# Performance work log

Hardware: AMD Instinct MI355X
Metric: run time of the kernel (lower is better)

## Reference

```python
import jax, jax.numpy as jnp
import numpy as np

N_NODES = 100000
N_EDGES = 1600000
IN_FEAT = 64
HIDDEN = 128
N_CLASSES = 16
N_GRAPHS = 512


def _glorot(key, shape):
    fan_in, fan_out = shape
    lim = (6.0 / (fan_in + fan_out)) ** 0.5
    return jax.random.uniform(key, shape, jnp.float32, -lim, lim)


def setup_inputs() -> dict:
    key = jax.random.key(0)
    ks = jax.random.split(key, 12)
    x = jax.random.normal(ks[0], (N_NODES, IN_FEAT), jnp.float32)
    edge_index = jax.random.randint(ks[1], (2, N_EDGES), 0, N_NODES, jnp.int64)
    batch = jnp.sort(jax.random.randint(ks[2], (N_NODES,), 0, N_GRAPHS, jnp.int64))
    # SAGEConv params: lin_l (neighbor agg, with bias), lin_r (root, no bias)
    params = {}
    dims = [(IN_FEAT, HIDDEN), (HIDDEN, HIDDEN), (HIDDEN, HIDDEN)]
    for i, (din, dout) in enumerate(dims, start=1):
        params[f"Wl{i}"] = _glorot(ks[2 + 2 * i - 1], (din, dout))
        params[f"bl{i}"] = jnp.zeros((dout,), jnp.float32)
        params[f"Wr{i}"] = _glorot(ks[2 + 2 * i], (din, dout))
    params["W_out"] = _glorot(ks[9], (HIDDEN, N_CLASSES))
    params["b_out"] = jnp.zeros((N_CLASSES,), jnp.float32)
    return {"x": x, "edge_index": edge_index, "batch": batch, **params}


def _sage_conv(x, src, dst, Wl, bl, Wr):
    # mean aggregation of neighbor (source) features onto target nodes
    msg = x[src]                                                # [E, D]
    agg_sum = jax.ops.segment_sum(msg, dst, num_segments=N_NODES)
    cnt = jax.ops.segment_sum(jnp.ones((src.shape[0],), x.dtype), dst,
                              num_segments=N_NODES)
    agg = agg_sum / jnp.maximum(cnt, 1.0)[:, None]
    return agg @ Wl + bl + x @ Wr


def reference(x, edge_index, batch, Wl1, bl1, Wr1, Wl2, bl2, Wr2,
              Wl3, bl3, Wr3, W_out, b_out):
    src, dst = edge_index[0], edge_index[1]
    h = jax.nn.relu(_sage_conv(x, src, dst, Wl1, bl1, Wr1))
    h = jax.nn.relu(_sage_conv(h, src, dst, Wl2, bl2, Wr2))
    h = _sage_conv(h, src, dst, Wl3, bl3, Wr3)
    # global mean pool over graphs
    g_sum = jax.ops.segment_sum(h, batch, num_segments=N_GRAPHS)
    g_cnt = jax.ops.segment_sum(jnp.ones((h.shape[0],), h.dtype), batch,
                                num_segments=N_GRAPHS)
    g = g_sum / jnp.maximum(g_cnt, 1.0)[:, None]
    # dropout is identity at inference (module.eval())
    return g @ W_out + b_out
```

## Files before the change

kernel.cpp:

```cpp
#include <hip/hip_runtime.h>

#define N_NODES   100000
#define N_PAD     100096
#define N_EDGES   1600000
#define IN_FEAT   64
#define HIDDEN    128
#define N_CLASSES 16
#define N_GRAPHS  512
#define MAXDEG    64

#define BIN_NODES 512
#define NBINS     196
#define N_NODES_B (NBINS * BIN_NODES)
#define BINCAP    9000
#define EPB       2048

typedef __attribute__((ext_vector_type(8))) unsigned short us8;
typedef __attribute__((ext_vector_type(8))) short s8v;
typedef __attribute__((ext_vector_type(4))) float f4v;

__device__ __forceinline__ unsigned short f2bf(float f) {
    unsigned u = __builtin_bit_cast(unsigned, f);
    unsigned r = u + 0x7FFFu + ((u >> 16) & 1u);
    return (unsigned short)(r >> 16);
}
__device__ __forceinline__ float bf2f(unsigned short h) {
    unsigned u = ((unsigned)h) << 16;
    return __builtin_bit_cast(float, u);
}
__device__ __forceinline__ void acc8(float* a, us8 v) {
#pragma unroll
    for (int e = 0; e < 8; e++) a[e] += bf2f(v[e]);
}


__global__ __launch_bounds__(512) void bin_kernel(const int* __restrict__ src,
                                                  const int* __restrict__ dst,
                                                  int* __restrict__ bin_cursor,
                                                  int2* __restrict__ binbuf) {
    __shared__ int hist[NBINS];
    __shared__ int base[NBINS];
    const int t = threadIdx.x;
    for (int i = t; i < NBINS; i += 512) hist[i] = 0;
    __syncthreads();

    const int e0 = blockIdx.x * EPB;
    int myb[4], mys[4], myd[4], myp[4];
#pragma unroll
    for (int j = 0; j < 4; j++) {
        int e = e0 + t + j * 512;
        if (e < N_EDGES) {
            myd[j] = dst[e];
            mys[j] = src[e];
            myb[j] = myd[j] >> 9;
        } else {
            myb[j] = -1; mys[j] = 0; myd[j] = 0;
        }
    }
#pragma unroll
    for (int j = 0; j < 4; j++)
        myp[j] = (myb[j] >= 0) ? atomicAdd(&hist[myb[j]], 1) : 0;
    __syncthreads();

    for (int i = t; i < NBINS; i += 512) {
        int h = hist[i];
        base[i] = (h > 0) ? atomicAdd(&bin_cursor[i], h) : 0;
    }
    __syncthreads();

#pragma unroll
    for (int j = 0; j < 4; j++) {
        if (myb[j] >= 0) {
            int pos = base[myb[j]] + myp[j];
            if (pos < BINCAP)
                binbuf[(size_t)myb[j] * BINCAP + pos] = make_int2(mys[j], myd[j]);
        }
    }
}


__global__ __launch_bounds__(512) void build_kernel(const int2* __restrict__ binbuf,
                                                    const int* __restrict__ bin_cursor,
                                                    int* __restrict__ cursor,
                                                    int* __restrict__ csr) {
    __shared__ int lcur[BIN_NODES];
    __shared__ int lcsr[BIN_NODES * MAXDEG];
    const int b = blockIdx.x, t = threadIdx.x;
    if (t < BIN_NODES) lcur[t] = 0;
    __syncthreads();

    int cnt = bin_cursor[b];
    if (cnt > BINCAP) cnt = BINCAP;
    const int2* __restrict__ eb = binbuf + (size_t)b * BINCAP;
    for (int i = t; i < cnt; i += 512) {
        int2 e = eb[i];
        int dl = e.y - b * BIN_NODES;
        int p = atomicAdd(&lcur[dl], 1);
        if (p < MAXDEG) lcsr[dl * MAXDEG + p] = e.x;
    }
    __syncthreads();

    int4* __restrict__ gout = reinterpret_cast<int4*>(csr + (size_t)b * BIN_NODES * MAXDEG);
    const int4* __restrict__ lin = reinterpret_cast<const int4*>(lcsr);
    for (int i = t; i < BIN_NODES * MAXDEG / 4; i += 512) gout[i] = lin[i];
    if (t < BIN_NODES) cursor[b * BIN_NODES + t] = lcur[t];
}


__global__ void convert_x_kernel(const float* __restrict__ x, ushort* __restrict__ xh) {
    const int flat = blockIdx.x * 256 + threadIdx.x;
    const int row = flat >> 3;
    us8 w;
    if (row < N_NODES) {
        const float* p = x + (size_t)flat * 8;
        float4 v0 = *reinterpret_cast<const float4*>(p);
        float4 v1 = *reinterpret_cast<const float4*>(p + 4);
        w[0] = f2bf(v0.x); w[1] = f2bf(v0.y); w[2] = f2bf(v0.z); w[3] = f2bf(v0.w);
        w[4] = f2bf(v1.x); w[5] = f2bf(v1.y); w[6] = f2bf(v1.z); w[7] = f2bf(v1.w);
    } else {
#pragma unroll
        for (int e = 0; e < 8; e++) w[e] = 0;
    }
    reinterpret_cast<us8*>(xh)[flat] = w;
}


__global__ void pack_weights_kernel(const float* __restrict__ s0, const float* __restrict__ s1,
                                    const float* __restrict__ s2, const float* __restrict__ s3,
                                    const float* __restrict__ s4, const float* __restrict__ s5,
                                    ushort* __restrict__ Bpk) {
    const int flat = blockIdx.x * 256 + threadIdx.x;
    const float* src; int base;
    if      (flat < 8192)  { src = s0; base = 0; }
    else if (flat < 16384) { src = s1; base = 8192; }
    else if (flat < 32768) { src = s2; base = 16384; }
    else if (flat < 49152) { src = s3; base = 32768; }
    else if (flat < 65536) { src = s4; base = 49152; }
    else                   { src = s5; base = 65536; }
    const int local = flat - base;
    const int j    = local & 7;
    const int lane = (local >> 3) & 63;
    const int tile = local >> 9;
    const int ks = tile >> 3, ct = tile & 7;
    const int row = ks * 32 + ((lane >> 4) << 3) + j;
    const int col = (ct << 4) + (lane & 15);
    Bpk[flat] = f2bf(src[row * 128 + col]);
}


template <int D>
__global__ __launch_bounds__(256, 4) void aggregate_bf(
        const ushort* __restrict__ feat, const int* __restrict__ cursor,
        const int* __restrict__ csr, ushort* __restrict__ aggout) {
    constexpr int LPN = D / 8;
    constexpr int NPB = 256 / LPN;
    const int tid  = threadIdx.x;
    const int lane = tid & (LPN - 1);
    const int n    = blockIdx.x * NPB + tid / LPN;
    if (n >= N_NODES) return;
    const int start = n * MAXDEG;
    int cnt = cursor[n];
    if (cnt > MAXDEG) cnt = MAXDEG;
    const us8* __restrict__ f8 = reinterpret_cast<const us8*>(feat);

    float a[8] = {0.f, 0.f, 0.f, 0.f, 0.f, 0.f, 0.f, 0.f};
    int i = 0;
    for (; i + 16 <= cnt; i += 16) {
        int t[16];
#pragma unroll
        for (int u = 0; u < 16; u++) t[u] = csr[start + i + u];
        us8 v[16];
#pragma unroll
        for (int u = 0; u < 16; u++) v[u] = f8[(size_t)t[u] * LPN + lane];
#pragma unroll
        for (int u = 0; u < 16; u++) acc8(a, v[u]);
    }
    for (; i + 8 <= cnt; i += 8) {
        int t[8];
#pragma unroll
        for (int u = 0; u < 8; u++) t[u] = csr[start + i + u];
        us8 v[8];
#pragma unroll
        for (int u = 0; u < 8; u++) v[u] = f8[(size_t)t[u] * LPN + lane];
#pragma unroll
        for (int u = 0; u < 8; u++) acc8(a, v[u]);
    }
    for (; i + 4 <= cnt; i += 4) {
        int t0 = csr[start + i + 0], t1 = csr[start + i + 1];
        int t2 = csr[start + i + 2], t3 = csr[start + i + 3];
        us8 v0 = f8[(size_t)t0 * LPN + lane];
        us8 v1 = f8[(size_t)t1 * LPN + lane];
        us8 v2 = f8[(size_t)t2 * LPN + lane];
        us8 v3 = f8[(size_t)t3 * LPN + lane];
        acc8(a, v0); acc8(a, v1); acc8(a, v2); acc8(a, v3);
    }
    for (; i < cnt; i++) {
        us8 v0 = f8[(size_t)csr[start + i] * LPN + lane];
        acc8(a, v0);
    }
    const float inv = 1.f / (float)(cnt > 0 ? cnt : 1);
    us8 w;
#pragma unroll
    for (int e = 0; e < 8; e++) w[e] = f2bf(a[e] * inv);
    reinterpret_cast<us8*>(aggout)[(size_t)n * LPN + lane] = w;
}


template <int K, bool RELU>
__global__ __launch_bounds__(256, 2) void gemm_mfma(
        const ushort* __restrict__ A1, const ushort* __restrict__ A2,
        const ushort* __restrict__ B1p, const ushort* __restrict__ B2p,
        const float* __restrict__ bias, ushort* __restrict__ out) {
    constexpr int KS = K / 32;
    __shared__ ushort Bs[2 * KS * 8 * 512];
    const int tid = threadIdx.x;
    {
        const us8* g1 = reinterpret_cast<const us8*>(B1p);
        const us8* g2 = reinterpret_cast<const us8*>(B2p);
        us8* l8 = reinterpret_cast<us8*>(Bs);
        constexpr int PH = KS * 512;
#pragma unroll
        for (int i = 0; i < 4 * KS; i++) {
            int c = i * 256 + tid;
            if (i < 2 * KS) l8[c] = g1[c];
            else            l8[c] = g2[c - PH];
        }
    }
    __syncthreads();

    const int wave = tid >> 6, lane = tid & 63;
    const int r0 = blockIdx.x * 128 + wave * 32;
    const size_t arow = (size_t)(r0 + (lane & 15));
    const int koff = (lane >> 4) << 3;

    f4v acc[2][8];
#pragma unroll
    for (int rt = 0; rt < 2; rt++)
#pragma unroll
        for (int ct = 0; ct < 8; ct++) acc[rt][ct] = (f4v){0.f, 0.f, 0.f, 0.f};

    const s8v* Bf = reinterpret_cast<const s8v*>(Bs);
#pragma unroll
    for (int ph = 0; ph < 2; ph++) {
        const ushort* __restrict__ A = ph ? A2 : A1;
#pragma unroll
        for (int ks = 0; ks < KS; ks++) {
            s8v a0 = *reinterpret_cast<const s8v*>(A + arow * K + ks * 32 + koff);
            s8v a1 = *reinterpret_cast<const s8v*>(A + (arow + 16) * K + ks * 32 + koff);
#pragma unroll
            for (int ct = 0; ct < 8; ct++) {
                s8v b = Bf[((ph * KS + ks) * 8 + ct) * 64 + lane];
                acc[0][ct] = __builtin_amdgcn_mfma_f32_16x16x32_bf16(a0, b, acc[0][ct], 0, 0, 0);
                acc[1][ct] = __builtin_amdgcn_mfma_f32_16x16x32_bf16(a1, b, acc[1][ct], 0, 0, 0);
            }
        }
    }

    const int colb = lane & 15;
    const int rowb = (lane >> 4) << 2;
#pragma unroll
    for (int rt = 0; rt < 2; rt++) {
#pragma unroll
        for (int ct = 0; ct < 8; ct++) {
            const int col = ct * 16 + colb;
            const float bb = bias[col];
#pragma unroll
            for (int j = 0; j < 4; j++) {
                int row = r0 + rt * 16 + rowb + j;
                if (row < N_NODES) {
                    float v = acc[rt][ct][j] + bb;
                    if (RELU) v = fmaxf(v, 0.f);
                    out[(size_t)row * HIDDEN + col] = f2bf(v);
                }
            }
        }
    }
}


__global__ __launch_bounds__(256) void pool_bf(const ushort* __restrict__ h,
                                               const int* __restrict__ batch,
                                               float* __restrict__ g) {
    __shared__ int sb[5];
    const int g0 = blockIdx.x * 4;
    const int tid = threadIdx.x;
    if (tid <= 4) {
        int target = g0 + tid;
        int lo = 0, hi = N_NODES;
        while (lo < hi) {
            int mid = (lo + hi) >> 1;
            if (batch[mid] < target) lo = mid + 1; else hi = mid;
        }
        sb[tid] = lo;
    }
    __syncthreads();
    const int lg = tid >> 6;
    const int lane = tid & 63;
    const int s = sb[lg], e = sb[lg + 1];
    const int nsub = lane >> 4;
    const int cc = lane & 15;
    const us8* __restrict__ h8 = reinterpret_cast<const us8*>(h);

    float a[8] = {0.f, 0.f, 0.f, 0.f, 0.f, 0.f, 0.f, 0.f};
    int n = s + nsub;
    for (; n + 12 < e; n += 16) {
        us8 v0 = h8[(size_t)(n + 0) * 16 + cc];
        us8 v1 = h8[(size_t)(n + 4) * 16 + cc];
        us8 v2 = h8[(size_t)(n + 8) * 16 + cc];
        us8 v3 = h8[(size_t)(n + 12) * 16 + cc];
        acc8(a, v0); acc8(a, v1); acc8(a, v2); acc8(a, v3);
    }
    for (; n < e; n += 4) {
        us8 v0 = h8[(size_t)n * 16 + cc];
        acc8(a, v0);
    }
#pragma unroll
    for (int e2 = 0; e2 < 8; e2++) {
        a[e2] += __shfl_xor(a[e2], 16);
        a[e2] += __shfl_xor(a[e2], 32);
    }
    if (nsub == 0) {
        const int cnt = e - s;
        const float inv = 1.f / (float)(cnt > 0 ? cnt : 1);
        float4 w0 = make_float4(a[0] * inv, a[1] * inv, a[2] * inv, a[3] * inv);
        float4 w1 = make_float4(a[4] * inv, a[5] * inv, a[6] * inv, a[7] * inv);
        float* dst = g + (size_t)(g0 + lg) * HIDDEN + cc * 8;
        *reinterpret_cast<float4*>(dst) = w0;
        *reinterpret_cast<float4*>(dst + 4) = w1;
    }
}


__global__ void head_kernel(const float* __restrict__ g, const float* __restrict__ W,
                            const float* __restrict__ b, float* __restrict__ out) {
    const int gid = blockIdx.x * 4 + (threadIdx.x >> 4);
    const int f = threadIdx.x & 15;
    if (gid >= N_GRAPHS) return;
    float acc = b[f];
    for (int k = 0; k < HIDDEN; k++)
        acc += g[(size_t)gid * HIDDEN + k] * W[k * N_CLASSES + f];
    out[(size_t)gid * N_CLASSES + f] = acc;
}


extern "C" void kernel_launch(void* const* d_in, const int* in_sizes, int n_in,
                              void* d_out, int out_size, void* d_ws, size_t ws_size,
                              hipStream_t stream) {
    const float* x    = (const float*)d_in[0];
    const int* eidx   = (const int*)d_in[1];
    const int* batch  = (const int*)d_in[2];
    const float* Wl1  = (const float*)d_in[3];
    const float* bl1  = (const float*)d_in[4];
    const float* Wr1  = (const float*)d_in[5];
    const float* Wl2  = (const float*)d_in[6];
    const float* bl2  = (const float*)d_in[7];
    const float* Wr2  = (const float*)d_in[8];
    const float* Wl3  = (const float*)d_in[9];
    const float* bl3  = (const float*)d_in[10];
    const float* Wr3  = (const float*)d_in[11];
    const float* Wout = (const float*)d_in[12];
    const float* bout = (const float*)d_in[13];
    float* out = (float*)d_out;

    const int* esrc = eidx;
    const int* edst = eidx + N_EDGES;

    char* ws = (char*)d_ws;
    size_t o = 0;
    int*  bin_cursor = (int*)(ws + o);  o += 256 * 4;
    int*  cursor     = (int*)(ws + o);  o += (size_t)N_NODES_B * 4;
    int*  csr        = (int*)(ws + o);  o += (size_t)N_NODES_B * MAXDEG * 4;
    int2* binbuf     = (int2*)(ws + o); o += (size_t)NBINS * BINCAP * 8;
    o = (o + 255) & ~(size_t)255;
    ushort* xh   = (ushort*)(ws + o); o += (size_t)N_PAD * IN_FEAT * 2;
    ushort* aggb = (ushort*)(ws + o); o += (size_t)N_PAD * HIDDEN * 2;
    ushort* h1b  = (ushort*)(ws + o); o += (size_t)N_PAD * HIDDEN * 2;
    ushort* h2b  = (ushort*)(ws + o); o += (size_t)N_PAD * HIDDEN * 2;
    ushort* Bpk  = (ushort*)(ws + o); o += (size_t)81920 * 2;
    float*  g    = (float*)(ws + o);  o += (size_t)N_GRAPHS * HIDDEN * 4;

    hipMemsetAsync(bin_cursor, 0, 256 * 4, stream);

    bin_kernel<<<(N_EDGES + EPB - 1) / EPB, 512, 0, stream>>>(esrc, edst, bin_cursor, binbuf);
    build_kernel<<<NBINS, 512, 0, stream>>>(binbuf, bin_cursor, cursor, csr);

    pack_weights_kernel<<<320, 256, 0, stream>>>(Wl1, Wr1, Wl2, Wr2, Wl3, Wr3, Bpk);
    convert_x_kernel<<<(N_PAD * IN_FEAT / 8) / 256, 256, 0, stream>>>(x, xh);

    ushort* Wl1p = Bpk + 0,     *Wr1p = Bpk + 8192;
    ushort* Wl2p = Bpk + 16384, *Wr2p = Bpk + 32768;
    ushort* Wl3p = Bpk + 49152, *Wr3p = Bpk + 65536;

    const int GB = N_PAD / 128;

    aggregate_bf<IN_FEAT><<<(N_NODES + 31) / 32, 256, 0, stream>>>(xh, cursor, csr, aggb);
    gemm_mfma<IN_FEAT, true><<<GB, 256, 0, stream>>>(aggb, xh, Wl1p, Wr1p, bl1, h1b);
    aggregate_bf<HIDDEN><<<(N_NODES + 15) / 16, 256, 0, stream>>>(h1b, cursor, csr, aggb);
    gemm_mfma<HIDDEN, true><<<GB, 256, 0, stream>>>(aggb, h1b, Wl2p, Wr2p, bl2, h2b);
    aggregate_bf<HIDDEN><<<(N_NODES + 15) / 16, 256, 0, stream>>>(h2b, cursor, csr, aggb);
    gemm_mfma<HIDDEN, false><<<GB, 256, 0, stream>>>(aggb, h2b, Wl3p, Wr3p, bl3, h1b);

    pool_bf<<<N_GRAPHS / 4, 256, 0, stream>>>(h1b, batch, g);
    head_kernel<<<N_GRAPHS / 4, 64, 0, stream>>>(g, Wout, bout, out);
}
```

Before: 372.8 us.

## Commute layer-3 linear map past mean pooling to skip per-node GEMM

Layer 3 has no ReLU, so its linear transform is moved after the graph mean pool. The new kernel pools the per-node neighbor means and the root features per graph, and the weights are applied only to 512 pooled vectors in a fused head kernel. This removes the full layer-3 aggregate write, the per-node GEMM and the pooled re-read of h. The cost is that the edge gather now runs inside the pooling kernel with a 4-way segment split per graph, plus some extra partial-sum buffers. The bias handling for empty graphs is adjusted to match the reference.

```diff
diff --git a/kernel.cpp b/kernel.cpp
--- a/kernel.cpp
+++ b/kernel.cpp
@@ -8,6 +8,7 @@
 #define N_CLASSES 16
 #define N_GRAPHS  512
 #define MAXDEG    64
+#define PSEG      4
 
 #define BIN_NODES 512
 #define NBINS     196
@@ -127,16 +128,13 @@
 
 __global__ void pack_weights_kernel(const float* __restrict__ s0, const float* __restrict__ s1,
                                     const float* __restrict__ s2, const float* __restrict__ s3,
-                                    const float* __restrict__ s4, const float* __restrict__ s5,
                                     ushort* __restrict__ Bpk) {
     const int flat = blockIdx.x * 256 + threadIdx.x;
     const float* src; int base;
     if      (flat < 8192)  { src = s0; base = 0; }
     else if (flat < 16384) { src = s1; base = 8192; }
     else if (flat < 32768) { src = s2; base = 16384; }
-    else if (flat < 49152) { src = s3; base = 32768; }
-    else if (flat < 65536) { src = s4; base = 49152; }
-    else                   { src = s5; base = 65536; }
+    else                   { src = s3; base = 32768; }
     const int local = flat - base;
     const int j    = local & 7;
     const int lane = (local >> 3) & 63;
@@ -278,14 +276,17 @@
 }
 
 
-__global__ __launch_bounds__(256) void pool_bf(const ushort* __restrict__ h,
-                                               const int* __restrict__ batch,
-                                               float* __restrict__ g) {
-    __shared__ int sb[5];
-    const int g0 = blockIdx.x * 4;
+__global__ __launch_bounds__(256) void edge_pool(
+        const ushort* __restrict__ h2, const int* __restrict__ batch,
+        const int* __restrict__ cursor, const int* __restrict__ csr,
+        float* __restrict__ Pe, float* __restrict__ Pn, int* __restrict__ gcnt) {
+    const int blk = blockIdx.x;
+    const int gid = blk >> 2, seg = blk & (PSEG - 1);
+    __shared__ int sb[2];
+    __shared__ float red[4][2][128];
     const int tid = threadIdx.x;
-    if (tid <= 4) {
-        int target = g0 + tid;
+    if (tid < 2) {
+        int target = gid + tid;
         int lo = 0, hi = N_NODES;
         while (lo < hi) {
             int mid = (lo + hi) >> 1;
@@ -294,52 +295,113 @@
         sb[tid] = lo;
     }
     __syncthreads();
-    const int lg = tid >> 6;
-    const int lane = tid & 63;
-    const int s = sb[lg], e = sb[lg + 1];
-    const int nsub = lane >> 4;
-    const int cc = lane & 15;
-    const us8* __restrict__ h8 = reinterpret_cast<const us8*>(h);
-
-    float a[8] = {0.f, 0.f, 0.f, 0.f, 0.f, 0.f, 0.f, 0.f};
-    int n = s + nsub;
-    for (; n + 12 < e; n += 16) {
-        us8 v0 = h8[(size_t)(n + 0) * 16 + cc];
-        us8 v1 = h8[(size_t)(n + 4) * 16 + cc];
-        us8 v2 = h8[(size_t)(n + 8) * 16 + cc];
-        us8 v3 = h8[(size_t)(n + 12) * 16 + cc];
-        acc8(a, v0); acc8(a, v1); acc8(a, v2); acc8(a, v3);
-    }
-    for (; n < e; n += 4) {
-        us8 v0 = h8[(size_t)n * 16 + cc];
-        acc8(a, v0);
-    }
-#pragma unroll
-    for (int e2 = 0; e2 < 8; e2++) {
-        a[e2] += __shfl_xor(a[e2], 16);
-        a[e2] += __shfl_xor(a[e2], 32);
-    }
-    if (nsub == 0) {
-        const int cnt = e - s;
+    const int s = sb[0], e = sb[1], len = e - s;
+    const int per = (len + PSEG - 1) / PSEG;
+    const int ss = s + seg * per;
+    int ee = ss + per; if (ee > e) ee = e;
+
+    const int ch  = tid & 15;
+    const int grp = tid >> 4;
+    const us8* __restrict__ f8 = reinterpret_cast<const us8*>(h2);
+    float pe[8] = {0.f, 0.f, 0.f, 0.f, 0.f, 0.f, 0.f, 0.f};
+    float pn[8] = {0.f, 0.f, 0.f, 0.f, 0.f, 0.f, 0.f, 0.f};
+
+    for (int n = ss + grp; n < ee; n += 16) {
+        const int start = n * MAXDEG;
+        int cnt = cursor[n];
+        if (cnt > MAXDEG) cnt = MAXDEG;
+        float a[8] = {0.f, 0.f, 0.f, 0.f, 0.f, 0.f, 0.f, 0.f};
+        int i = 0;
+        for (; i + 8 <= cnt; i += 8) {
+            int t0 = csr[start + i + 0], t1 = csr[start + i + 1];
+            int t2 = csr[start + i + 2], t3 = csr[start + i + 3];
+            int t4 = csr[start + i + 4], t5 = csr[start + i + 5];
+            int t6 = csr[start + i + 6], t7 = csr[start + i + 7];
+            us8 v0 = f8[(size_t)t0 * 16 + ch];
+            us8 v1 = f8[(size_t)t1 * 16 + ch];
+            us8 v2 = f8[(size_t)t2 * 16 + ch];
+            us8 v3 = f8[(size_t)t3 * 16 + ch];
+            us8 v4 = f8[(size_t)t4 * 16 + ch];
+            us8 v5 = f8[(size_t)t5 * 16 + ch];
+            us8 v6 = f8[(size_t)t6 * 16 + ch];
+            us8 v7 = f8[(size_t)t7 * 16 + ch];
+            acc8(a, v0); acc8(a, v1); acc8(a, v2); acc8(a, v3);
+            acc8(a, v4); acc8(a, v5); acc8(a, v6); acc8(a, v7);
+        }
+        for (; i + 4 <= cnt; i += 4) {
+            int t0 = csr[start + i + 0], t1 = csr[start + i + 1];
+            int t2 = csr[start + i + 2], t3 = csr[start + i + 3];
+            us8 v0 = f8[(size_t)t0 * 16 + ch];
+            us8 v1 = f8[(size_t)t1 * 16 + ch];
+            us8 v2 = f8[(size_t)t2 * 16 + ch];
+            us8 v3 = f8[(size_t)t3 * 16 + ch];
+            acc8(a, v0); acc8(a, v1); acc8(a, v2); acc8(a, v3);
+        }
+        for (; i < cnt; i++) {
+            us8 v0 = f8[(size_t)csr[start + i] * 16 + ch];
+            acc8(a, v0);
+        }
         const float inv = 1.f / (float)(cnt > 0 ? cnt : 1);
-        float4 w0 = make_float4(a[0] * inv, a[1] * inv, a[2] * inv, a[3] * inv);
-        float4 w1 = make_float4(a[4] * inv, a[5] * inv, a[6] * inv, a[7] * inv);
-        float* dst = g + (size_t)(g0 + lg) * HIDDEN + cc * 8;
-        *reinterpret_cast<float4*>(dst) = w0;
-        *reinterpret_cast<float4*>(dst + 4) = w1;
-    }
-}
-
-
-__global__ void head_kernel(const float* __restrict__ g, const float* __restrict__ W,
-                            const float* __restrict__ b, float* __restrict__ out) {
-    const int gid = blockIdx.x * 4 + (threadIdx.x >> 4);
-    const int f = threadIdx.x & 15;
-    if (gid >= N_GRAPHS) return;
-    float acc = b[f];
-    for (int k = 0; k < HIDDEN; k++)
-        acc += g[(size_t)gid * HIDDEN + k] * W[k * N_CLASSES + f];
-    out[(size_t)gid * N_CLASSES + f] = acc;
+#pragma unroll
+        for (int j = 0; j < 8; j++) pe[j] += a[j] * inv;
+        us8 v = f8[(size_t)n * 16 + ch];
+        acc8(pn, v);
+    }
+
+#pragma unroll
+    for (int j = 0; j < 8; j++) {
+        pe[j] += __shfl_xor(pe[j], 16); pe[j] += __shfl_xor(pe[j], 32);
+        pn[j] += __shfl_xor(pn[j], 16); pn[j] += __shfl_xor(pn[j], 32);
+    }
+    const int wave = tid >> 6, lane = tid & 63;
+    if (lane < 16) {
+#pragma unroll
+        for (int j = 0; j < 8; j++) {
+            red[wave][0][lane * 8 + j] = pe[j];
+            red[wave][1][lane * 8 + j] = pn[j];
+        }
+    }
+    __syncthreads();
+    if (tid < 128) {
+        float se = red[0][0][tid] + red[1][0][tid] + red[2][0][tid] + red[3][0][tid];
+        float sn = red[0][1][tid] + red[1][1][tid] + red[2][1][tid] + red[3][1][tid];
+        Pe[(size_t)blk * 128 + tid] = se;
+        Pn[(size_t)blk * 128 + tid] = sn;
+    }
+    if (tid == 0 && seg == 0) gcnt[gid] = len;
+}
+
+
+__global__ __launch_bounds__(128) void head_fused(
+        const float* __restrict__ Pe, const float* __restrict__ Pn,
+        const int* __restrict__ gcnt,
+        const float* __restrict__ Wl3, const float* __restrict__ Wr3,
+        const float* __restrict__ bl3,
+        const float* __restrict__ Wout, const float* __restrict__ bout,
+        float* __restrict__ out) {
+    const int gid = blockIdx.x, c = threadIdx.x;
+    __shared__ float lse[128], lsn[128], lg[128];
+    float se = 0.f, sn = 0.f;
+#pragma unroll
+    for (int sg = 0; sg < PSEG; sg++) {
+        se += Pe[(size_t)(gid * PSEG + sg) * 128 + c];
+        sn += Pn[(size_t)(gid * PSEG + sg) * 128 + c];
+    }
+    const int len = gcnt[gid];
+    const float inv = 1.f / (float)(len > 0 ? len : 1);
+    lse[c] = se * inv;
+    lsn[c] = sn * inv;
+    __syncthreads();
+    float acc = (len > 0) ? bl3[c] : 0.f;
+    for (int k = 0; k < 128; k++)
+        acc += lse[k] * Wl3[k * 128 + c] + lsn[k] * Wr3[k * 128 + c];
+    lg[c] = acc;
+    __syncthreads();
+    if (c < N_CLASSES) {
+        float o = bout[c];
+        for (int k = 0; k < 128; k++) o += lg[k] * Wout[k * N_CLASSES + c];
+        out[(size_t)gid * N_CLASSES + c] = o;
+    }
 }
 
 
@@ -376,20 +438,21 @@
     ushort* aggb = (ushort*)(ws + o); o += (size_t)N_PAD * HIDDEN * 2;
     ushort* h1b  = (ushort*)(ws + o); o += (size_t)N_PAD * HIDDEN * 2;
     ushort* h2b  = (ushort*)(ws + o); o += (size_t)N_PAD * HIDDEN * 2;
-    ushort* Bpk  = (ushort*)(ws + o); o += (size_t)81920 * 2;
-    float*  g    = (float*)(ws + o);  o += (size_t)N_GRAPHS * HIDDEN * 4;
+    ushort* Bpk  = (ushort*)(ws + o); o += (size_t)49152 * 2;
+    float*  Pe   = (float*)(ws + o);  o += (size_t)N_GRAPHS * PSEG * 128 * 4;
+    float*  Pn   = (float*)(ws + o);  o += (size_t)N_GRAPHS * PSEG * 128 * 4;
+    int*    gcnt = (int*)(ws + o);    o += (size_t)N_GRAPHS * 4;
 
     hipMemsetAsync(bin_cursor, 0, 256 * 4, stream);
 
     bin_kernel<<<(N_EDGES + EPB - 1) / EPB, 512, 0, stream>>>(esrc, edst, bin_cursor, binbuf);
     build_kernel<<<NBINS, 512, 0, stream>>>(binbuf, bin_cursor, cursor, csr);
 
-    pack_weights_kernel<<<320, 256, 0, stream>>>(Wl1, Wr1, Wl2, Wr2, Wl3, Wr3, Bpk);
+    pack_weights_kernel<<<192, 256, 0, stream>>>(Wl1, Wr1, Wl2, Wr2, Bpk);
     convert_x_kernel<<<(N_PAD * IN_FEAT / 8) / 256, 256, 0, stream>>>(x, xh);
 
     ushort* Wl1p = Bpk + 0,     *Wr1p = Bpk + 8192;
     ushort* Wl2p = Bpk + 16384, *Wr2p = Bpk + 32768;
-    ushort* Wl3p = Bpk + 49152, *Wr3p = Bpk + 65536;
 
     const int GB = N_PAD / 128;
 
@@ -397,9 +460,6 @@
     gemm_mfma<IN_FEAT, true><<<GB, 256, 0, stream>>>(aggb, xh, Wl1p, Wr1p, bl1, h1b);
     aggregate_bf<HIDDEN><<<(N_NODES + 15) / 16, 256, 0, stream>>>(h1b, cursor, csr, aggb);
     gemm_mfma<HIDDEN, true><<<GB, 256, 0, stream>>>(aggb, h1b, Wl2p, Wr2p, bl2, h2b);
-    aggregate_bf<HIDDEN><<<(N_NODES + 15) / 16, 256, 0, stream>>>(h2b, cursor, csr, aggb);
-    gemm_mfma<HIDDEN, false><<<GB, 256, 0, stream>>>(aggb, h2b, Wl3p, Wr3p, bl3, h1b);
-
-    pool_bf<<<N_GRAPHS / 4, 256, 0, stream>>>(h1b, batch, g);
-    head_kernel<<<N_GRAPHS / 4, 64, 0, stream>>>(g, Wout, bout, out);
-}
+    edge_pool<<<N_GRAPHS * PSEG, 256, 0, stream>>>(h2b, batch, cursor, csr, Pe, Pn, gcnt);
+    head_fused<<<N_GRAPHS, 128, 0, stream>>>(Pe, Pn, gcnt, Wl3, Wr3, bl3, Wout, bout, out);
+}
```

Measured after the change: 351.3 us. 5.8% less time.
